# Kernel optimization log

Hardware: AMD Instinct MI355X
Metric: run time of the kernel (lower is better)

## Reference

```python
import jax, jax.numpy as jnp
import numpy as np

N_NODES = 100000
N_EDGES = 300000
D = 256
EPS = 1e-5
ALPHA = 0.5  # residual_alpha


def setup_inputs() -> dict:
    key = jax.random.key(0)
    ks = jax.random.split(key, 6)
    x = jax.random.normal(ks[0], (N_NODES, D), dtype=jnp.float32)
    edge_index = jax.random.randint(ks[1], (2, N_EDGES), 0, N_NODES, dtype=jnp.int32)
    edge_weight = jax.random.uniform(ks[2], (N_EDGES,), dtype=jnp.float32)
    # GCNConv parameters (glorot-ish weight, bias)
    W = jax.random.normal(ks[3], (D, D), dtype=jnp.float32) / np.float32(np.sqrt(D))
    b = 0.01 * jax.random.normal(ks[4], (D,), dtype=jnp.float32)
    # LayerNorm parameters
    gamma = jnp.ones((D,), dtype=jnp.float32)
    beta = jnp.zeros((D,), dtype=jnp.float32)
    return {"x": x, "edge_index": edge_index, "edge_weight": edge_weight,
            "W": W, "b": b, "gamma": gamma, "beta": beta}


def gcn_residual(x, edge_index, edge_weight, W, b, gamma, beta):
    src, dst = edge_index[0], edge_index[1]
    # linear transform first (PyG GCNConv order)
    h = x @ W  # [N, D]
    # gcn_norm with added self-loops (self-loop weight = 1)
    deg = jax.ops.segment_sum(edge_weight, dst, num_segments=N_NODES) + 1.0  # [N]
    dinv = jax.lax.rsqrt(deg)
    norm = dinv[src] * edge_weight * dinv[dst]  # [E]
    # message + aggregate (scatter-add over destination nodes)
    agg = jax.ops.segment_sum(norm[:, None] * h[src], dst, num_segments=N_NODES)
    agg = agg + (dinv * dinv)[:, None] * h  # self-loop contribution
    h = agg + b
    # LayerNorm over feature dim
    mu = jnp.mean(h, axis=-1, keepdims=True)
    var = jnp.mean(jnp.square(h - mu), axis=-1, keepdims=True)
    h = (h - mu) * jax.lax.rsqrt(var + EPS) * gamma + beta
    # dropout p=0.0 -> identity; weighted residual; relu
    h = ALPHA * h + (1.0 - ALPHA) * x
    return jax.nn.relu(h)


def reference(x, edge_index, edge_weight, W, b, gamma, beta):
    return gcn_residual(x, edge_index, edge_weight, W, b, gamma, beta)
```

## Files before the change

kernel.cpp:

```cpp
#include <hip/hip_runtime.h>


#define NN 100000
#define NE 300000
#define DD 256
#define NB 391
#define GMB 3125

typedef __attribute__((ext_vector_type(8))) short short8;
typedef __attribute__((ext_vector_type(4))) float f32x4;
typedef __attribute__((ext_vector_type(4))) unsigned short u16x4;

static __device__ __forceinline__ short f2bf(float f) {
  union { float f; unsigned u; } a; a.f = f;
  unsigned r = a.u + 0x7fffu + ((a.u >> 16) & 1u);
  return (short)(r >> 16);
}

static __device__ __forceinline__ float bf2f(short s) {
  return __uint_as_float((unsigned)(unsigned short)s << 16);
}

static __device__ __forceinline__ unsigned cvtpk(float a, float b) {
  unsigned r;
  asm("v_cvt_pk_bf16_f32 %0, %1, %2" : "=v"(r) : "v"(a), "v"(b));
  return r;
}

static __device__ __forceinline__ void gld16(const float* g, void* l) {
  __builtin_amdgcn_global_load_lds(
      (const __attribute__((address_space(1))) unsigned int*)g,
      (__attribute__((address_space(3))) unsigned int*)l, 16, 0, 0);
}

__global__ __launch_bounds__(256) void k_init(float* __restrict__ dv,
                                              int* __restrict__ cnt) {
  int i = blockIdx.x * 256 + threadIdx.x;
  if (i < NN) { dv[i] = 0.0f; cnt[i] = 0; }
}

__global__ __launch_bounds__(256) void k_hist(const int* __restrict__ ei,
                                              const float* __restrict__ ew,
                                              float* __restrict__ dv,
                                              int* __restrict__ cnt) {
  int e = blockIdx.x * 256 + threadIdx.x;
  if (e < NE) {
    int d = ei[NE + e];
    atomicAdd(&dv[d], ew[e]);
    atomicAdd(&cnt[d], 1);
  }
}

__global__ __launch_bounds__(256) void k_scan1(const int* __restrict__ cnt,
                                               int* __restrict__ off,
                                               int* __restrict__ bsum) {
  __shared__ int tmp[256];
  int t = threadIdx.x;
  int i = blockIdx.x * 256 + t;
  int v = (i < NN) ? cnt[i] : 0;
  tmp[t] = v;
  __syncthreads();
  for (int o = 1; o < 256; o <<= 1) {
    int u = (t >= o) ? tmp[t - o] : 0;
    __syncthreads();
    tmp[t] += u;
    __syncthreads();
  }
  if (i < NN) off[i] = tmp[t] - v;
  if (t == 255) bsum[blockIdx.x] = tmp[t];
}

__global__ __launch_bounds__(512) void k_scan2(int* __restrict__ bsum) {
  __shared__ int tmp[512];
  int t = threadIdx.x;
  int v = (t < NB) ? bsum[t] : 0;
  tmp[t] = v;
  __syncthreads();
  for (int o = 1; o < 512; o <<= 1) {
    int u = (t >= o) ? tmp[t - o] : 0;
    __syncthreads();
    tmp[t] += u;
    __syncthreads();
  }
  bsum[t] = tmp[t] - v;
}

__global__ __launch_bounds__(256) void k_scan3(int* __restrict__ off,
                                               const int* __restrict__ bsum,
                                               int* __restrict__ cur,
                                               float* __restrict__ dv) {
  int i = blockIdx.x * 256 + threadIdx.x;
  if (i < NN) {
    int o = off[i] + bsum[i >> 8];
    off[i] = o;
    cur[i] = o;
    dv[i] = rsqrtf(dv[i] + 1.0f);
  }
}

__global__ __launch_bounds__(256) void k_place(const int* __restrict__ ei,
                                               const float* __restrict__ ew,
                                               const float* __restrict__ dv,
                                               int* __restrict__ cur,
                                               int2* __restrict__ elist) {
  int e = blockIdx.x * 256 + threadIdx.x;
  if (e >= NE) return;
  int s = ei[e];
  int d = ei[NE + e];
  float c = dv[s] * ew[e] * dv[d];
  int pos = atomicAdd(&cur[d], 1);
  elist[pos] = make_int2(s, __float_as_int(c));
}

__global__ __launch_bounds__(256) void k_wprep(const float* __restrict__ W,
                                               short* __restrict__ Wf) {
  int idx = blockIdx.x * 256 + threadIdx.x;
  int k = idx >> 6;
  int c4 = idx & 63;
  const float4 v = *(const float4*)(W + k * 256 + c4 * 4);
  float vv[4] = {v.x, v.y, v.z, v.w};
#pragma unroll
  for (int i = 0; i < 4; ++i) {
    int c = c4 * 4 + i;
    int di = ((k >> 5) * 16 + (c >> 4)) * 512 + ((c & 15) + ((k >> 3) & 3) * 16) * 8 + (k & 7);
    Wf[di] = f2bf(vv[i]);
  }
}

__global__ __launch_bounds__(256) void k_gemm(const float* __restrict__ x,
                                              const short* __restrict__ Wf,
                                              short* __restrict__ h) {
  __shared__ float As[32 * 256];

  const int t = threadIdx.x;
  const int lane = t & 63;
  const int wid = t >> 6;
  const int row0 = blockIdx.x * 32;

#pragma unroll
  for (int i = 0; i < 8; ++i) {
    const int r = i * 4 + wid;
    const float* src = x + (size_t)(row0 + r) * 256 + ((lane ^ (r & 7)) << 2);
    gld16(src, (char*)As + (r << 10));
  }
  __syncthreads();

  f32x4 acc[4][2];
#pragma unroll
  for (int mc = 0; mc < 4; ++mc)
#pragma unroll
    for (int nr = 0; nr < 2; ++nr) acc[mc][nr] = (f32x4)0.0f;

  const short* wbase = Wf + (size_t)(wid * 4) * 512 + lane * 8;

#pragma unroll
  for (int ks = 0; ks < 8; ++ks) {
    short8 bx[2];
#pragma unroll
    for (int nr = 0; nr < 2; ++nr) {
      const int r = nr * 16 + (lane & 15);
      const int c = ks * 8 + (lane >> 4) * 2;
      const f32x4 lo = *(const f32x4*)((const char*)As + (r << 10) + ((c ^ (r & 7)) << 4));
      const f32x4 hi = *(const f32x4*)((const char*)As + (r << 10) + (((c + 1) ^ (r & 7)) << 4));
      union { short8 s; unsigned u[4]; } U;
      U.u[0] = cvtpk(lo[0], lo[1]);
      U.u[1] = cvtpk(lo[2], lo[3]);
      U.u[2] = cvtpk(hi[0], hi[1]);
      U.u[3] = cvtpk(hi[2], hi[3]);
      bx[nr] = U.s;
    }
    short8 aw[4];
#pragma unroll
    for (int mc = 0; mc < 4; ++mc)
      aw[mc] = *(const short8*)(wbase + (size_t)(ks * 16 + mc) * 512);
#pragma unroll
    for (int mc = 0; mc < 4; ++mc)
#pragma unroll
      for (int nr = 0; nr < 2; ++nr)
        acc[mc][nr] = __builtin_amdgcn_mfma_f32_16x16x32_bf16(
            aw[mc], bx[nr], acc[mc][nr], 0, 0, 0);
  }

#pragma unroll
  for (int mc = 0; mc < 4; ++mc) {
    const int cbase = wid * 64 + mc * 16 + 4 * (lane >> 4);
#pragma unroll
    for (int nr = 0; nr < 2; ++nr) {
      const int r = row0 + nr * 16 + (lane & 15);
      u16x4 s;
      s[0] = (unsigned short)f2bf(acc[mc][nr][0]);
      s[1] = (unsigned short)f2bf(acc[mc][nr][1]);
      s[2] = (unsigned short)f2bf(acc[mc][nr][2]);
      s[3] = (unsigned short)f2bf(acc[mc][nr][3]);
      *(u16x4*)(h + (size_t)r * 256 + cbase) = s;
    }
  }
}

__global__ __launch_bounds__(256) void k_agg(const short* __restrict__ h,
                                             const float* __restrict__ dv,
                                             const int* __restrict__ cnt,
                                             const int* __restrict__ off,
                                             const int2* __restrict__ elist,
                                             const float* __restrict__ x,
                                             const float* __restrict__ b,
                                             const float* __restrict__ gamma,
                                             const float* __restrict__ beta,
                                             float* __restrict__ out) {
  int node = (blockIdx.x * 256 + threadIdx.x) >> 5;
  if (node >= NN) return;
  int q = threadIdx.x & 31;

  const float di = dv[node];
  const float d2 = di * di;
  short8 hv = *(const short8*)(h + (size_t)node * 256 + q * 8);
  float a[8];
#pragma unroll
  for (int i = 0; i < 8; ++i) a[i] = bf2f(hv[i]) * d2;

  const int n = cnt[node];
  const int st = off[node];
  int j = 0;
  for (; j + 4 <= n; j += 4) {
    int2 r0 = elist[st + j];
    int2 r1 = elist[st + j + 1];
    int2 r2 = elist[st + j + 2];
    int2 r3 = elist[st + j + 3];
    short8 g0 = *(const short8*)(h + (size_t)r0.x * 256 + q * 8);
    short8 g1 = *(const short8*)(h + (size_t)r1.x * 256 + q * 8);
    short8 g2 = *(const short8*)(h + (size_t)r2.x * 256 + q * 8);
    short8 g3 = *(const short8*)(h + (size_t)r3.x * 256 + q * 8);
    float c0 = __int_as_float(r0.y);
    float c1 = __int_as_float(r1.y);
    float c2 = __int_as_float(r2.y);
    float c3 = __int_as_float(r3.y);
#pragma unroll
    for (int i = 0; i < 8; ++i)
      a[i] += c0 * bf2f(g0[i]) + c1 * bf2f(g1[i]) + c2 * bf2f(g2[i]) + c3 * bf2f(g3[i]);
  }
  for (; j < n; ++j) {
    int2 r0 = elist[st + j];
    short8 g0 = *(const short8*)(h + (size_t)r0.x * 256 + q * 8);
    float c0 = __int_as_float(r0.y);
#pragma unroll
    for (int i = 0; i < 8; ++i) a[i] += c0 * bf2f(g0[i]);
  }

  const float4 b0 = *(const float4*)(b + q * 8);
  const float4 b1 = *(const float4*)(b + q * 8 + 4);
  a[0] += b0.x; a[1] += b0.y; a[2] += b0.z; a[3] += b0.w;
  a[4] += b1.x; a[5] += b1.y; a[6] += b1.z; a[7] += b1.w;

  float s = 0.f, ss = 0.f;
#pragma unroll
  for (int i = 0; i < 8; ++i) { s += a[i]; ss += a[i] * a[i]; }
#pragma unroll
  for (int o = 16; o > 0; o >>= 1) {
    s += __shfl_xor(s, o);
    ss += __shfl_xor(ss, o);
  }
  const float mu = s * (1.0f / 256.0f);
  const float var = ss * (1.0f / 256.0f) - mu * mu;
  const float inv = rsqrtf(var + 1e-5f);

  const float4 g0 = *(const float4*)(gamma + q * 8);
  const float4 g1 = *(const float4*)(gamma + q * 8 + 4);
  const float4 e0 = *(const float4*)(beta + q * 8);
  const float4 e1 = *(const float4*)(beta + q * 8 + 4);
  const float4 x0 = *(const float4*)(x + (size_t)node * 256 + q * 8);
  const float4 x1 = *(const float4*)(x + (size_t)node * 256 + q * 8 + 4);

  float4 r0, r1;
  r0.x = fmaxf(0.5f * ((a[0] - mu) * inv * g0.x + e0.x) + 0.5f * x0.x, 0.f);
  r0.y = fmaxf(0.5f * ((a[1] - mu) * inv * g0.y + e0.y) + 0.5f * x0.y, 0.f);
  r0.z = fmaxf(0.5f * ((a[2] - mu) * inv * g0.z + e0.z) + 0.5f * x0.z, 0.f);
  r0.w = fmaxf(0.5f * ((a[3] - mu) * inv * g0.w + e0.w) + 0.5f * x0.w, 0.f);
  r1.x = fmaxf(0.5f * ((a[4] - mu) * inv * g1.x + e1.x) + 0.5f * x1.x, 0.f);
  r1.y = fmaxf(0.5f * ((a[5] - mu) * inv * g1.y + e1.y) + 0.5f * x1.y, 0.f);
  r1.z = fmaxf(0.5f * ((a[6] - mu) * inv * g1.z + e1.z) + 0.5f * x1.z, 0.f);
  r1.w = fmaxf(0.5f * ((a[7] - mu) * inv * g1.w + e1.w) + 0.5f * x1.w, 0.f);

  float* o = out + (size_t)node * 256 + q * 8;
  *(float4*)(o) = r0;
  *(float4*)(o + 4) = r1;
}

extern "C" void kernel_launch(void* const* d_in, const int* in_sizes, int n_in,
                              void* d_out, int out_size, void* d_ws, size_t ws_size,
                              hipStream_t stream) {
  const float* x     = (const float*)d_in[0];
  const int*   ei    = (const int*)d_in[1];
  const float* ew    = (const float*)d_in[2];
  const float* W     = (const float*)d_in[3];
  const float* b     = (const float*)d_in[4];
  const float* gamma = (const float*)d_in[5];
  const float* beta  = (const float*)d_in[6];
  float* out = (float*)d_out;

  short* h   = (short*)d_ws;
  float* dv  = (float*)(h + (size_t)NN * DD);
  int*   cnt = (int*)(dv + NN);
  int*   off = cnt + NN;
  int*   cur = off + NN;
  int*   bsum = cur + NN;
  int2*  elist = (int2*)(bsum + 512);
  short* Wf  = (short*)(elist + NE);

  k_init<<<NB, 256, 0, stream>>>(dv, cnt);
  k_hist<<<(NE + 255) / 256, 256, 0, stream>>>(ei, ew, dv, cnt);
  k_scan1<<<NB, 256, 0, stream>>>(cnt, off, bsum);
  k_scan2<<<1, 512, 0, stream>>>(bsum);
  k_scan3<<<NB, 256, 0, stream>>>(off, bsum, cur, dv);
  k_place<<<(NE + 255) / 256, 256, 0, stream>>>(ei, ew, dv, cur, elist);

  k_wprep<<<64, 256, 0, stream>>>(W, Wf);
  k_gemm<<<GMB, 256, 0, stream>>>(x, Wf, h);

  k_agg<<<(NN * 32 + 255) / 256, 256, 0, stream>>>(h, dv, cnt, off, elist, x, b, gamma, beta, out);
}
```

Baseline: 167.1 us.

## Make GEMM blocks persistent over five tiles with double-buffered LDS prefetch

Each GEMM block now handles five 32-row tiles instead of one. The launch is reduced accordingly, and the bf16 W fragments are loaded into registers once per block rather than on every k-step. The x tile for the next iteration is prefetched into a second LDS buffer with async global-to-LDS loads while the current tile runs through MFMA, so load latency is meant to overlap compute. The cost is much higher register pressure (32 short8 W fragments held live) and twice the LDS. Occupancy is capped at two blocks per CU, and the vmcnt wait count is hand-tuned.

```diff
diff --git a/kernel.cpp b/kernel.cpp
--- a/kernel.cpp
+++ b/kernel.cpp
@@ -5,7 +5,7 @@
 #define NE 300000
 #define DD 256
 #define NB 391
-#define GMB 3125
+#define GMB 625
 
 typedef __attribute__((ext_vector_type(8))) short short8;
 typedef __attribute__((ext_vector_type(4))) float f32x4;
@@ -127,74 +127,93 @@
   }
 }
 
-__global__ __launch_bounds__(256) void k_gemm(const float* __restrict__ x,
-                                              const short* __restrict__ Wf,
-                                              short* __restrict__ h) {
-  __shared__ float As[32 * 256];
+__global__ __launch_bounds__(256, 2) void k_gemm(const float* __restrict__ x,
+                                                 const short* __restrict__ Wf,
+                                                 short* __restrict__ h) {
+  __shared__ float As[2][32 * 256];
 
   const int t = threadIdx.x;
   const int lane = t & 63;
   const int wid = t >> 6;
-  const int row0 = blockIdx.x * 32;
-
-#pragma unroll
-  for (int i = 0; i < 8; ++i) {
-    const int r = i * 4 + wid;
-    const float* src = x + (size_t)(row0 + r) * 256 + ((lane ^ (r & 7)) << 2);
-    gld16(src, (char*)As + (r << 10));
-  }
-  __syncthreads();
-
-  f32x4 acc[4][2];
-#pragma unroll
-  for (int mc = 0; mc < 4; ++mc)
-#pragma unroll
-    for (int nr = 0; nr < 2; ++nr) acc[mc][nr] = (f32x4)0.0f;
-
+  const int tile0 = blockIdx.x * 5;
+
+  short8 aw[8][4];
   const short* wbase = Wf + (size_t)(wid * 4) * 512 + lane * 8;
-
-#pragma unroll
-  for (int ks = 0; ks < 8; ++ks) {
-    short8 bx[2];
-#pragma unroll
-    for (int nr = 0; nr < 2; ++nr) {
-      const int r = nr * 16 + (lane & 15);
-      const int c = ks * 8 + (lane >> 4) * 2;
-      const f32x4 lo = *(const f32x4*)((const char*)As + (r << 10) + ((c ^ (r & 7)) << 4));
-      const f32x4 hi = *(const f32x4*)((const char*)As + (r << 10) + (((c + 1) ^ (r & 7)) << 4));
-      union { short8 s; unsigned u[4]; } U;
-      U.u[0] = cvtpk(lo[0], lo[1]);
-      U.u[1] = cvtpk(lo[2], lo[3]);
-      U.u[2] = cvtpk(hi[0], hi[1]);
-      U.u[3] = cvtpk(hi[2], hi[3]);
-      bx[nr] = U.s;
+#pragma unroll
+  for (int ks = 0; ks < 8; ++ks)
+#pragma unroll
+    for (int mc = 0; mc < 4; ++mc)
+      aw[ks][mc] = *(const short8*)(wbase + (size_t)(ks * 16 + mc) * 512);
+
+#define STAGE(T, B)                                                          \
+  _Pragma("unroll")                                                          \
+  for (int i = 0; i < 8; ++i) {                                              \
+    const int r_ = i * 4 + wid;                                              \
+    const float* src_ = x + ((size_t)(tile0 + (T)) * 32 + r_) * 256 +        \
+                        ((lane ^ (r_ & 7)) << 2);                            \
+    gld16(src_, (char*)As[B] + (r_ << 10));                                  \
+  }
+
+  STAGE(0, 0);
+
+#pragma unroll
+  for (int tt = 0; tt < 5; ++tt) {
+    const int cur = tt & 1;
+    if (tt < 4) { STAGE(tt + 1, cur ^ 1); }
+
+    asm volatile("s_waitcnt vmcnt(8)" ::: "memory");
+    __builtin_amdgcn_s_barrier();
+    __builtin_amdgcn_sched_barrier(0);
+
+    f32x4 acc[4][2];
+#pragma unroll
+    for (int mc = 0; mc < 4; ++mc)
+#pragma unroll
+      for (int nr = 0; nr < 2; ++nr) acc[mc][nr] = (f32x4)0.0f;
+
+#pragma unroll
+    for (int ks = 0; ks < 8; ++ks) {
+      short8 bx[2];
+#pragma unroll
+      for (int nr = 0; nr < 2; ++nr) {
+        const int r = nr * 16 + (lane & 15);
+        const int c = ks * 8 + (lane >> 4) * 2;
+        const f32x4 lo = *(const f32x4*)((const char*)As[cur] + (r << 10) + ((c ^ (r & 7)) << 4));
+        const f32x4 hi = *(const f32x4*)((const char*)As[cur] + (r << 10) + (((c + 1) ^ (r & 7)) << 4));
+        union { short8 s; unsigned u[4]; } U;
+        U.u[0] = cvtpk(lo[0], lo[1]);
+        U.u[1] = cvtpk(lo[2], lo[3]);
+        U.u[2] = cvtpk(hi[0], hi[1]);
+        U.u[3] = cvtpk(hi[2], hi[3]);
+        bx[nr] = U.s;
+      }
+#pragma unroll
+      for (int mc = 0; mc < 4; ++mc)
+#pragma unroll
+        for (int nr = 0; nr < 2; ++nr)
+          acc[mc][nr] = __builtin_amdgcn_mfma_f32_16x16x32_bf16(
+              aw[ks][mc], bx[nr], acc[mc][nr], 0, 0, 0);
     }
-    short8 aw[4];
-#pragma unroll
-    for (int mc = 0; mc < 4; ++mc)
-      aw[mc] = *(const short8*)(wbase + (size_t)(ks * 16 + mc) * 512);
-#pragma unroll
-    for (int mc = 0; mc < 4; ++mc)
-#pragma unroll
-      for (int nr = 0; nr < 2; ++nr)
-        acc[mc][nr] = __builtin_amdgcn_mfma_f32_16x16x32_bf16(
-            aw[mc], bx[nr], acc[mc][nr], 0, 0, 0);
-  }
-
-#pragma unroll
-  for (int mc = 0; mc < 4; ++mc) {
-    const int cbase = wid * 64 + mc * 16 + 4 * (lane >> 4);
-#pragma unroll
-    for (int nr = 0; nr < 2; ++nr) {
-      const int r = row0 + nr * 16 + (lane & 15);
-      u16x4 s;
-      s[0] = (unsigned short)f2bf(acc[mc][nr][0]);
-      s[1] = (unsigned short)f2bf(acc[mc][nr][1]);
-      s[2] = (unsigned short)f2bf(acc[mc][nr][2]);
-      s[3] = (unsigned short)f2bf(acc[mc][nr][3]);
-      *(u16x4*)(h + (size_t)r * 256 + cbase) = s;
+
+    __builtin_amdgcn_s_barrier();
+
+    const int rowb = (tile0 + tt) * 32;
+#pragma unroll
+    for (int mc = 0; mc < 4; ++mc) {
+      const int cbase = wid * 64 + mc * 16 + 4 * (lane >> 4);
+#pragma unroll
+      for (int nr = 0; nr < 2; ++nr) {
+        const int r = rowb + nr * 16 + (lane & 15);
+        u16x4 s;
+        s[0] = (unsigned short)f2bf(acc[mc][nr][0]);
+        s[1] = (unsigned short)f2bf(acc[mc][nr][1]);
+        s[2] = (unsigned short)f2bf(acc[mc][nr][2]);
+        s[3] = (unsigned short)f2bf(acc[mc][nr][3]);
+        *(u16x4*)(h + (size_t)r * 256 + cbase) = s;
+      }
     }
   }
+#undef STAGE
 }
 
 __global__ __launch_bounds__(256) void k_agg(const short* __restrict__ h,
```

After: 153.2 us. 8.3% less time.
